# Kernel optimization log

Hardware: AMD Instinct MI355X
Metric: run time of the kernel (lower is better)

The kernel has to match this reference:

```python
import jax, jax.numpy as jnp
import numpy as np

RADIUS = 0.5
HEADS = 4
LATENT = 128
KIN = 3 + 3 + 3 + 1  # q_pos + o_pos + rel + dist
LN_EPS = 1e-5


def setup_inputs() -> dict:
    key = jax.random.key(0)
    ks = jax.random.split(key, 12)
    B, Nq, No = 2, 1024, 1024
    h_obs = jax.random.normal(ks[0], (B, No, LATENT), dtype=jnp.float32)
    pos_obs = jax.random.uniform(ks[1], (B, No, 3), dtype=jnp.float32)
    pos_query = jax.random.uniform(ks[2], (B, Nq, 3), dtype=jnp.float32)
    obs_mask = jax.random.randint(ks[3], (B, No), 0, 2, dtype=jnp.int32)
    # kernel MLP params: Linear(KIN, LATENT) -> ReLU -> Linear(LATENT, HEADS)
    W1 = jax.random.normal(ks[4], (KIN, LATENT), dtype=jnp.float32) * (1.0 / np.sqrt(KIN))
    b1 = jax.random.normal(ks[5], (LATENT,), dtype=jnp.float32) * 0.01
    W2 = jax.random.normal(ks[6], (LATENT, HEADS), dtype=jnp.float32) * (1.0 / np.sqrt(LATENT))
    b2 = jax.random.normal(ks[7], (HEADS,), dtype=jnp.float32) * 0.01
    ln_g = jnp.ones((LATENT,), dtype=jnp.float32)
    ln_b = jnp.zeros((LATENT,), dtype=jnp.float32)
    Wv = jax.random.normal(ks[8], (LATENT, LATENT), dtype=jnp.float32) * (1.0 / np.sqrt(LATENT))
    bv = jax.random.normal(ks[9], (LATENT,), dtype=jnp.float32) * 0.01
    return {"h_obs": h_obs, "pos_obs": pos_obs, "pos_query": pos_query,
            "obs_mask": obs_mask, "W1": W1, "b1": b1, "W2": W2, "b2": b2,
            "ln_g": ln_g, "ln_b": ln_b, "Wv": Wv, "bv": bv}


def reference(h_obs, pos_obs, pos_query, obs_mask, W1, b1, W2, b2, ln_g, ln_b, Wv, bv):
    B, Nq, _ = pos_query.shape
    _, No, _ = pos_obs.shape
    H, D = HEADS, LATENT // HEADS

    # pairwise geometric encoding: (B, Nq, No, *)
    rel = pos_query[:, :, None, :] - pos_obs[:, None, :, :]
    dist = jnp.linalg.norm(rel, axis=-1, keepdims=True)
    q_exp = jnp.broadcast_to(pos_query[:, :, None, :], rel.shape)
    o_exp = jnp.broadcast_to(pos_obs[:, None, :, :], rel.shape)
    kin = jnp.concatenate([q_exp, o_exp, rel, dist], axis=-1)  # (B,Nq,No,KIN)

    # per-pair MLP -> per-head attention logits
    hid = jax.nn.relu(kin @ W1 + b1)                 # (B,Nq,No,LATENT)
    logits = hid @ W2 + b2                           # (B,Nq,No,H)
    logits = jnp.transpose(logits, (0, 3, 1, 2))     # (B,H,Nq,No)

    # radius + observation masking
    neg = jnp.float32(-jnp.inf)
    mask = (dist[..., 0] > RADIUS)[:, None, :, :] | (obs_mask == 0)[:, None, None, :]
    logits = jnp.where(mask, neg, logits)
    weights = jax.nn.softmax(logits, axis=-1)        # (B,H,Nq,No)

    # value path: LayerNorm + projection
    mu = jnp.mean(h_obs, axis=-1, keepdims=True)
    var = jnp.var(h_obs, axis=-1, keepdims=True)
    hn = (h_obs - mu) / jnp.sqrt(var + LN_EPS) * ln_g + ln_b
    v = hn @ Wv + bv                                 # (B,No,LATENT)
    v = jnp.transpose(v.reshape(B, No, H, D), (0, 2, 1, 3))  # (B,H,No,D)

    out = jnp.einsum('bhqo,bhod->bhqd', weights, v)  # (B,H,Nq,D)
    out = jnp.transpose(out, (0, 2, 1, 3)).reshape(B, Nq, H * D)
    return out
```

## Files before the change

### kernel.cpp

```cpp
#include <hip/hip_runtime.h>
#include <math.h>
#include <float.h>

#define B_ 2
#define NQ 1024
#define NO 1024
#define LAT 128
#define NHEADS 4
#define RADIUS_ 0.5f
#define LN_EPS_ 1e-5f

#define V_BYTES ((size_t)B_ * NO * LAT * 4)

__global__ __launch_bounds__(128) void gano_prep_kernel(
    const float* __restrict__ h_obs, const float* __restrict__ ln_g,
    const float* __restrict__ ln_b, const float* __restrict__ Wv,
    const float* __restrict__ bv, const float* __restrict__ W1,
    const float* __restrict__ b1, float* __restrict__ v_out,
    float4* __restrict__ Cw, float4* __restrict__ A4, int write_derived)
{
  const int r = blockIdx.x;
  const int j = threadIdx.x;
  __shared__ float s_red[2];
  __shared__ __align__(16) float s_hn[LAT];

  const float x = h_obs[(size_t)r * LAT + j];

  float s = x;
  #pragma unroll
  for (int off = 32; off >= 1; off >>= 1) s += __shfl_down(s, off);
  if ((j & 63) == 0) s_red[j >> 6] = s;
  __syncthreads();
  const float mu = (s_red[0] + s_red[1]) * (1.0f / LAT);
  const float d = x - mu;
  __syncthreads();
  float s2 = d * d;
  #pragma unroll
  for (int off = 32; off >= 1; off >>= 1) s2 += __shfl_down(s2, off);
  if ((j & 63) == 0) s_red[j >> 6] = s2;
  __syncthreads();
  const float var = (s_red[0] + s_red[1]) * (1.0f / LAT);
  const float rstd = rsqrtf(var + LN_EPS_);
  s_hn[j] = d * rstd * ln_g[j] + ln_b[j];
  __syncthreads();

  float acc = bv[j];
  const float4* hn4 = (const float4*)s_hn;
  #pragma unroll 4
  for (int k4 = 0; k4 < LAT / 4; ++k4) {
    const float4 h4 = hn4[k4];
    acc = fmaf(h4.x, Wv[(k4 * 4 + 0) * LAT + j], acc);
    acc = fmaf(h4.y, Wv[(k4 * 4 + 1) * LAT + j], acc);
    acc = fmaf(h4.z, Wv[(k4 * 4 + 2) * LAT + j], acc);
    acc = fmaf(h4.w, Wv[(k4 * 4 + 3) * LAT + j], acc);
  }
  v_out[(size_t)r * LAT + j] = acc;

  if (write_derived && r == 0) {
    float w[10];
    #pragma unroll
    for (int k = 0; k < 10; ++k) w[k] = W1[k * LAT + j];
    Cw[j] = make_float4(w[3] - w[6], w[4] - w[7], w[5] - w[8], w[9]);
    A4[j] = make_float4(w[0] + w[6], w[1] + w[7], w[2] + w[8], b1[j]);
  }
}

template <bool DERIVED>
__global__ __launch_bounds__(256, 8) void gano_main_kernel(
    const float* __restrict__ pos_obs, const float* __restrict__ pos_query,
    const int* __restrict__ obs_mask,
    const float* __restrict__ W1, const float* __restrict__ b1,
    const float4* __restrict__ W2v, const float* __restrict__ b2,
    const float* __restrict__ v,
    const float4* __restrict__ Cw, const float4* __restrict__ A4,
    float* __restrict__ out)
{
  __shared__ __align__(16) float s_Q[LAT];
  __shared__ int   s_vidx[NO];
  __shared__ float s_vdist[NO];
  __shared__ float s_p[NHEADS][256];
  __shared__ int   s_cnt[16];
  __shared__ float s_red[NHEADS][4];
  __shared__ float s_m[NHEADS];
  __shared__ float s_z[NHEADS];
  __shared__ float s_scale[NHEADS];
  __shared__ float s_acc[LAT];

  const int tid = threadIdx.x;
  const int wave = tid >> 6, lane = tid & 63;
  const int bid = blockIdx.x;
  const int b = bid >> 10, q = bid & (NQ - 1);

  const float qx = pos_query[((size_t)b * NQ + q) * 3 + 0];
  const float qy = pos_query[((size_t)b * NQ + q) * 3 + 1];
  const float qz = pos_query[((size_t)b * NQ + q) * 3 + 2];

  if (tid < LAT) {
    float a0, a1, a2, a3;
    if constexpr (DERIVED) {
      const float4 a = A4[tid];
      a0 = a.x; a1 = a.y; a2 = a.z; a3 = a.w;
    } else {
      a0 = W1[0 * LAT + tid] + W1[6 * LAT + tid];
      a1 = W1[1 * LAT + tid] + W1[7 * LAT + tid];
      a2 = W1[2 * LAT + tid] + W1[8 * LAT + tid];
      a3 = b1[tid];
    }
    s_Q[tid] = fmaf(qx, a0, fmaf(qy, a1, fmaf(qz, a2, a3)));
  }
  if (tid < NHEADS) { s_m[tid] = -FLT_MAX; s_z[tid] = 0.0f; }

  const float* pob = pos_obs + (size_t)b * NO * 3;
  const int*   om  = obs_mask + (size_t)b * NO;
  float dists[4];
  unsigned long long bals[4];
  #pragma unroll
  for (int rd = 0; rd < 4; ++rd) {
    const int o = (rd << 8) + tid;
    const float ox = pob[o * 3 + 0], oy = pob[o * 3 + 1], oz = pob[o * 3 + 2];
    const float rx = qx - ox, ry = qy - oy, rz = qz - oz;
    const float dist = sqrtf(rx * rx + ry * ry + rz * rz);
    const int ok = (om[o] != 0) && (dist <= RADIUS_);
    const unsigned long long bal = __ballot(ok);
    if (lane == 0) s_cnt[(rd << 2) + wave] = __popcll(bal);
    bals[rd] = bal;
    dists[rd] = dist;
  }
  __syncthreads();
  int Nv = 0;
  #pragma unroll
  for (int k = 0; k < 16; ++k) Nv += s_cnt[k];
  #pragma unroll
  for (int rd = 0; rd < 4; ++rd) {
    const int slot = (rd << 2) + wave;
    int base = 0;
    for (int k = 0; k < slot; ++k) base += s_cnt[k];
    if ((bals[rd] >> lane) & 1ull) {
      const int pos = base + __popcll(bals[rd] & ((1ull << lane) - 1ull));
      s_vidx[pos] = (rd << 8) + tid;
      s_vdist[pos] = dists[rd];
    }
  }
  __syncthreads();

  const int col = tid & (LAT - 1);
  const int half = tid >> 7;
  const int hh = col >> 5;
  float acc = 0.0f;
  const float* vb = v + (size_t)b * NO * LAT;
  const float b20 = b2[0], b21 = b2[1], b22 = b2[2], b23 = b2[3];

  const int ntiles = (Nv + 255) >> 8;
  for (int tile = 0; tile < ntiles; ++tile) {
    const int tbase = tile << 8;
    const int t = tbase + tid;
    const bool active = t < Nv;
    float l0 = -FLT_MAX, l1 = -FLT_MAX, l2 = -FLT_MAX, l3 = -FLT_MAX;
    if (__any(active)) {
      const int tt = active ? t : (Nv - 1);
      const int idx = s_vidx[tt];
      const float dist = s_vdist[tt];
      const float ox = pob[idx * 3 + 0], oy = pob[idx * 3 + 1], oz = pob[idx * 3 + 2];
      float a0 = b20, a1 = b21, a2 = b22, a3 = b23;
      for (int j4 = 0; j4 < LAT / 4; ++j4) {
        const float4 q4 = *(const float4*)&s_Q[j4 << 2];
        #pragma unroll
        for (int u = 0; u < 4; ++u) {
          const int j = (j4 << 2) + u;
          float4 cw;
          if constexpr (DERIVED) {
            cw = Cw[j];
          } else {
            cw = make_float4(W1[3 * LAT + j] - W1[6 * LAT + j],
                             W1[4 * LAT + j] - W1[7 * LAT + j],
                             W1[5 * LAT + j] - W1[8 * LAT + j],
                             W1[9 * LAT + j]);
          }
          const float4 w2 = W2v[j];
          const float qj = (u == 0) ? q4.x : (u == 1) ? q4.y : (u == 2) ? q4.z : q4.w;
          float t0 = fmaf(cw.x, ox, qj);
          t0 = fmaf(cw.y, oy, t0);
          t0 = fmaf(cw.z, oz, t0);
          t0 = fmaf(cw.w, dist, t0);
          t0 = fmaxf(t0, 0.0f);
          a0 = fmaf(t0, w2.x, a0);
          a1 = fmaf(t0, w2.y, a1);
          a2 = fmaf(t0, w2.z, a2);
          a3 = fmaf(t0, w2.w, a3);
        }
      }
      if (active) { l0 = a0; l1 = a1; l2 = a2; l3 = a3; }
    }

    float m0 = l0, m1 = l1, m2 = l2, m3 = l3;
    #pragma unroll
    for (int off = 32; off >= 1; off >>= 1) {
      m0 = fmaxf(m0, __shfl_down(m0, off));
      m1 = fmaxf(m1, __shfl_down(m1, off));
      m2 = fmaxf(m2, __shfl_down(m2, off));
      m3 = fmaxf(m3, __shfl_down(m3, off));
    }
    if (lane == 0) { s_red[0][wave] = m0; s_red[1][wave] = m1;
                     s_red[2][wave] = m2; s_red[3][wave] = m3; }
    __syncthreads();
    if (tid < NHEADS) {
      const float tm = fmaxf(fmaxf(s_red[tid][0], s_red[tid][1]),
                             fmaxf(s_red[tid][2], s_red[tid][3]));
      const float om_ = s_m[tid];
      const float nm = fmaxf(om_, tm);
      s_scale[tid] = __expf(om_ - nm);
      s_m[tid] = nm;
    }
    __syncthreads();
    const float nm0 = s_m[0], nm1 = s_m[1], nm2 = s_m[2], nm3 = s_m[3];
    const float p0 = __expf(l0 - nm0);
    const float p1 = __expf(l1 - nm1);
    const float p2 = __expf(l2 - nm2);
    const float p3 = __expf(l3 - nm3);
    s_p[0][tid] = p0; s_p[1][tid] = p1; s_p[2][tid] = p2; s_p[3][tid] = p3;
    float z0 = p0, z1 = p1, z2 = p2, z3 = p3;
    #pragma unroll
    for (int off = 32; off >= 1; off >>= 1) {
      z0 += __shfl_down(z0, off);
      z1 += __shfl_down(z1, off);
      z2 += __shfl_down(z2, off);
      z3 += __shfl_down(z3, off);
    }
    if (lane == 0) { s_red[0][wave] = z0; s_red[1][wave] = z1;
                     s_red[2][wave] = z2; s_red[3][wave] = z3; }
    acc *= s_scale[hh];
    __syncthreads();
    if (tid < NHEADS) {
      s_z[tid] = s_z[tid] * s_scale[tid] +
                 (s_red[tid][0] + s_red[tid][1] + s_red[tid][2] + s_red[tid][3]);
    }
    const int tcnt = min(256, Nv - tbase);
    float aa0 = 0.0f, aa1 = 0.0f;
    int u2 = half;
    for (; u2 + 2 < tcnt; u2 += 4) {
      const float pA = s_p[hh][u2];
      const float pB = s_p[hh][u2 + 2];
      const int iA = s_vidx[tbase + u2];
      const int iB = s_vidx[tbase + u2 + 2];
      aa0 = fmaf(pA, vb[iA * LAT + col], aa0);
      aa1 = fmaf(pB, vb[iB * LAT + col], aa1);
    }
    for (; u2 < tcnt; u2 += 2)
      aa0 = fmaf(s_p[hh][u2], vb[s_vidx[tbase + u2] * LAT + col], aa0);
    acc += aa0 + aa1;
    __syncthreads();
  }

  if (half) s_acc[col] = acc;
  __syncthreads();
  if (!half) {
    float r = 0.0f;
    if (Nv > 0) r = (acc + s_acc[col]) / s_z[hh];
    out[((size_t)b * NQ + q) * LAT + col] = r;
  }
}

extern "C" void kernel_launch(void* const* d_in, const int* in_sizes, int n_in,
                              void* d_out, int out_size, void* d_ws, size_t ws_size,
                              hipStream_t stream) {
  const float* h_obs     = (const float*)d_in[0];
  const float* pos_obs   = (const float*)d_in[1];
  const float* pos_query = (const float*)d_in[2];
  const int*   obs_mask  = (const int*)d_in[3];
  const float* W1        = (const float*)d_in[4];
  const float* b1        = (const float*)d_in[5];
  const float* W2        = (const float*)d_in[6];
  const float* b2        = (const float*)d_in[7];
  const float* ln_g      = (const float*)d_in[8];
  const float* ln_b      = (const float*)d_in[9];
  const float* Wv        = (const float*)d_in[10];
  const float* bv        = (const float*)d_in[11];
  float* outp = (float*)d_out;
  float* v    = (float*)d_ws;

  const size_t need = V_BYTES + 2 * LAT * sizeof(float4);
  const int derived = (ws_size >= need) ? 1 : 0;
  float4* Cw = (float4*)((char*)d_ws + V_BYTES);
  float4* A4 = Cw + LAT;
  if (!derived) { Cw = (float4*)d_ws; A4 = (float4*)d_ws; }

  gano_prep_kernel<<<B_ * NO, 128, 0, stream>>>(h_obs, ln_g, ln_b, Wv, bv,
                                                W1, b1, v, Cw, A4, derived);
  if (derived) {
    gano_main_kernel<true><<<B_ * NQ, 256, 0, stream>>>(
        pos_obs, pos_query, obs_mask, W1, b1, (const float4*)W2, b2, v,
        (const float4*)Cw, (const float4*)A4, outp);
  } else {
    gano_main_kernel<false><<<B_ * NQ, 256, 0, stream>>>(
        pos_obs, pos_query, obs_mask, W1, b1, (const float4*)W2, b2, v,
        (const float4*)Cw, (const float4*)A4, outp);
  }
}
```

Measured before the change: 48.19 us.

## Enlarge softmax tile, vectorize value gather, keep stats in registers, batch LN rows

New measurement: 39.36 us. 18.3% less time.

```diff
diff --git a/kernel.cpp b/kernel.cpp
--- a/kernel.cpp
+++ b/kernel.cpp
@@ -9,64 +9,139 @@
 #define NHEADS 4
 #define RADIUS_ 0.5f
 #define LN_EPS_ 1e-5f
+#define TILE 512
+#define TILE_P (TILE + 8)
 
 #define V_BYTES ((size_t)B_ * NO * LAT * 4)
 
-__global__ __launch_bounds__(128) void gano_prep_kernel(
+__device__ __forceinline__ float selh(int h, float a, float b, float c, float d) {
+  return h == 0 ? a : (h == 1 ? b : (h == 2 ? c : d));
+}
+
+__global__ __launch_bounds__(256) void gano_prep_kernel(
     const float* __restrict__ h_obs, const float* __restrict__ ln_g,
     const float* __restrict__ ln_b, const float* __restrict__ Wv,
     const float* __restrict__ bv, const float* __restrict__ W1,
     const float* __restrict__ b1, float* __restrict__ v_out,
     float4* __restrict__ Cw, float4* __restrict__ A4, int write_derived)
 {
-  const int r = blockIdx.x;
-  const int j = threadIdx.x;
-  __shared__ float s_red[2];
-  __shared__ __align__(16) float s_hn[LAT];
-
-  const float x = h_obs[(size_t)r * LAT + j];
-
-  float s = x;
-  #pragma unroll
-  for (int off = 32; off >= 1; off >>= 1) s += __shfl_down(s, off);
-  if ((j & 63) == 0) s_red[j >> 6] = s;
-  __syncthreads();
-  const float mu = (s_red[0] + s_red[1]) * (1.0f / LAT);
-  const float d = x - mu;
-  __syncthreads();
-  float s2 = d * d;
-  #pragma unroll
-  for (int off = 32; off >= 1; off >>= 1) s2 += __shfl_down(s2, off);
-  if ((j & 63) == 0) s_red[j >> 6] = s2;
-  __syncthreads();
-  const float var = (s_red[0] + s_red[1]) * (1.0f / LAT);
-  const float rstd = rsqrtf(var + LN_EPS_);
-  s_hn[j] = d * rstd * ln_g[j] + ln_b[j];
-  __syncthreads();
-
-  float acc = bv[j];
-  const float4* hn4 = (const float4*)s_hn;
+  const int tid = threadIdx.x;
+  const int j = tid & 127;
+  const int half = tid >> 7;
+  const int wave = tid >> 6;
+  const int lane = tid & 63;
+  const int r0 = blockIdx.x * 4 + half * 2;
+
+  __shared__ float s_redA[2][4];
+  __shared__ float s_redB[2][4];
+  __shared__ __align__(16) float s_hn[4][LAT];
+
+  const float x0 = h_obs[(size_t)r0 * LAT + j];
+  const float x1 = h_obs[(size_t)(r0 + 1) * LAT + j];
+  float s0 = x0, s1 = x1;
+  #pragma unroll
+  for (int off = 32; off >= 1; off >>= 1) {
+    s0 += __shfl_down(s0, off);
+    s1 += __shfl_down(s1, off);
+  }
+  if (lane == 0) { s_redA[0][wave] = s0; s_redA[1][wave] = s1; }
+  __syncthreads();
+  const float mu0 = (s_redA[0][half * 2] + s_redA[0][half * 2 + 1]) * (1.0f / LAT);
+  const float mu1 = (s_redA[1][half * 2] + s_redA[1][half * 2 + 1]) * (1.0f / LAT);
+  const float d0 = x0 - mu0, d1 = x1 - mu1;
+  float q0 = d0 * d0, q1 = d1 * d1;
+  #pragma unroll
+  for (int off = 32; off >= 1; off >>= 1) {
+    q0 += __shfl_down(q0, off);
+    q1 += __shfl_down(q1, off);
+  }
+  if (lane == 0) { s_redB[0][wave] = q0; s_redB[1][wave] = q1; }
+  __syncthreads();
+  const float var0 = (s_redB[0][half * 2] + s_redB[0][half * 2 + 1]) * (1.0f / LAT);
+  const float var1 = (s_redB[1][half * 2] + s_redB[1][half * 2 + 1]) * (1.0f / LAT);
+  const float g = ln_g[j], be = ln_b[j];
+  s_hn[half * 2 + 0][j] = d0 * rsqrtf(var0 + LN_EPS_) * g + be;
+  s_hn[half * 2 + 1][j] = d1 * rsqrtf(var1 + LN_EPS_) * g + be;
+  __syncthreads();
+
+  float a0 = 0.0f, a1 = 0.0f;
+  const float4* h0 = (const float4*)s_hn[half * 2 + 0];
+  const float4* h1 = (const float4*)s_hn[half * 2 + 1];
   #pragma unroll 4
   for (int k4 = 0; k4 < LAT / 4; ++k4) {
-    const float4 h4 = hn4[k4];
-    acc = fmaf(h4.x, Wv[(k4 * 4 + 0) * LAT + j], acc);
-    acc = fmaf(h4.y, Wv[(k4 * 4 + 1) * LAT + j], acc);
-    acc = fmaf(h4.z, Wv[(k4 * 4 + 2) * LAT + j], acc);
-    acc = fmaf(h4.w, Wv[(k4 * 4 + 3) * LAT + j], acc);
-  }
-  v_out[(size_t)r * LAT + j] = acc;
-
-  if (write_derived && r == 0) {
+    const float4 u0 = h0[k4];
+    const float4 u1 = h1[k4];
+    const float w0 = Wv[(k4 * 4 + 0) * LAT + j];
+    const float w1 = Wv[(k4 * 4 + 1) * LAT + j];
+    const float w2 = Wv[(k4 * 4 + 2) * LAT + j];
+    const float w3 = Wv[(k4 * 4 + 3) * LAT + j];
+    a0 = fmaf(u0.x, w0, a0); a0 = fmaf(u0.y, w1, a0);
+    a0 = fmaf(u0.z, w2, a0); a0 = fmaf(u0.w, w3, a0);
+    a1 = fmaf(u1.x, w0, a1); a1 = fmaf(u1.y, w1, a1);
+    a1 = fmaf(u1.z, w2, a1); a1 = fmaf(u1.w, w3, a1);
+  }
+  const float bvj = bv[j];
+  v_out[(size_t)(r0 + 0) * LAT + j] = a0 + bvj;
+  v_out[(size_t)(r0 + 1) * LAT + j] = a1 + bvj;
+
+  if (write_derived && blockIdx.x == 0 && tid < LAT) {
     float w[10];
     #pragma unroll
-    for (int k = 0; k < 10; ++k) w[k] = W1[k * LAT + j];
-    Cw[j] = make_float4(w[3] - w[6], w[4] - w[7], w[5] - w[8], w[9]);
-    A4[j] = make_float4(w[0] + w[6], w[1] + w[7], w[2] + w[8], b1[j]);
+    for (int k = 0; k < 10; ++k) w[k] = W1[k * LAT + tid];
+    Cw[tid] = make_float4(w[3] - w[6], w[4] - w[7], w[5] - w[8], w[9]);
+    A4[tid] = make_float4(w[0] + w[6], w[1] + w[7], w[2] + w[8], b1[tid]);
   }
 }
 
 template <bool DERIVED>
-__global__ __launch_bounds__(256, 8) void gano_main_kernel(
+__device__ __forceinline__ void mlp_logits(
+    int t, int Nv, const float* s_Q, const int* s_vidx, const float* s_vdist,
+    const float* __restrict__ pob, const float4* __restrict__ Cw,
+    const float4* __restrict__ W2v, const float* __restrict__ W1,
+    float b20, float b21, float b22, float b23,
+    float& l0, float& l1, float& l2, float& l3)
+{
+  const bool active = t < Nv;
+  l0 = l1 = l2 = l3 = -FLT_MAX;
+  if (!__any(active)) return;
+  const int tt = active ? t : Nv - 1;
+  const int idx = s_vidx[tt];
+  const float dist = s_vdist[tt];
+  const float ox = pob[idx * 3 + 0], oy = pob[idx * 3 + 1], oz = pob[idx * 3 + 2];
+  float a0 = b20, a1 = b21, a2 = b22, a3 = b23;
+  #pragma unroll 2
+  for (int j4 = 0; j4 < LAT / 4; ++j4) {
+    const float4 q4 = *(const float4*)&s_Q[j4 << 2];
+    #pragma unroll
+    for (int u = 0; u < 4; ++u) {
+      const int jj = (j4 << 2) + u;
+      float4 cw;
+      if constexpr (DERIVED) {
+        cw = Cw[jj];
+      } else {
+        cw = make_float4(W1[3 * LAT + jj] - W1[6 * LAT + jj],
+                         W1[4 * LAT + jj] - W1[7 * LAT + jj],
+                         W1[5 * LAT + jj] - W1[8 * LAT + jj],
+                         W1[9 * LAT + jj]);
+      }
+      const float4 w2 = W2v[jj];
+      const float qj = (u == 0) ? q4.x : (u == 1) ? q4.y : (u == 2) ? q4.z : q4.w;
+      float gg = fmaf(cw.x, ox, qj);
+      gg = fmaf(cw.y, oy, gg);
+      gg = fmaf(cw.z, oz, gg);
+      gg = fmaf(cw.w, dist, gg);
+      gg = fmaxf(gg, 0.0f);
+      a0 = fmaf(gg, w2.x, a0);
+      a1 = fmaf(gg, w2.y, a1);
+      a2 = fmaf(gg, w2.z, a2);
+      a3 = fmaf(gg, w2.w, a3);
+    }
+  }
+  if (active) { l0 = a0; l1 = a1; l2 = a2; l3 = a3; }
+}
+
+template <bool DERIVED>
+__global__ __launch_bounds__(256, 6) void gano_main_kernel(
     const float* __restrict__ pos_obs, const float* __restrict__ pos_query,
     const int* __restrict__ obs_mask,
     const float* __restrict__ W1, const float* __restrict__ b1,
@@ -78,13 +153,11 @@
   __shared__ __align__(16) float s_Q[LAT];
   __shared__ int   s_vidx[NO];
   __shared__ float s_vdist[NO];
-  __shared__ float s_p[NHEADS][256];
+  __shared__ float s_p[NHEADS][TILE_P];
   __shared__ int   s_cnt[16];
   __shared__ float s_red[NHEADS][4];
-  __shared__ float s_m[NHEADS];
-  __shared__ float s_z[NHEADS];
-  __shared__ float s_scale[NHEADS];
-  __shared__ float s_acc[LAT];
+  __shared__ float s_zred[NHEADS][4];
+  __shared__ __align__(16) float s_part[4][LAT];
 
   const int tid = threadIdx.x;
   const int wave = tid >> 6, lane = tid & 63;
@@ -108,7 +181,6 @@
     }
     s_Q[tid] = fmaf(qx, a0, fmaf(qy, a1, fmaf(qz, a2, a3)));
   }
-  if (tid < NHEADS) { s_m[tid] = -FLT_MAX; s_z[tid] = 0.0f; }
 
   const float* pob = pos_obs + (size_t)b * NO * 3;
   const int*   om  = obs_mask + (size_t)b * NO;
@@ -143,120 +215,113 @@
   }
   __syncthreads();
 
-  const int col = tid & (LAT - 1);
-  const int half = tid >> 7;
-  const int hh = col >> 5;
-  float acc = 0.0f;
+  const int c5 = tid & 31;
+  const int phase = tid >> 5;
+  const int hh = c5 >> 3;
+  float ax = 0.f, ay = 0.f, az = 0.f, aw = 0.f;
+  float m0 = -FLT_MAX, m1 = -FLT_MAX, m2 = -FLT_MAX, m3 = -FLT_MAX;
+  float z0 = 0.f, z1 = 0.f, z2 = 0.f, z3 = 0.f;
+  const float b20 = b2[0], b21 = b2[1], b22 = b2[2], b23 = b2[3];
   const float* vb = v + (size_t)b * NO * LAT;
-  const float b20 = b2[0], b21 = b2[1], b22 = b2[2], b23 = b2[3];
-
-  const int ntiles = (Nv + 255) >> 8;
+  const float* vcol = vb + (c5 << 2);
+
+  const int ntiles = (Nv + TILE - 1) >> 9;
   for (int tile = 0; tile < ntiles; ++tile) {
-    const int tbase = tile << 8;
-    const int t = tbase + tid;
-    const bool active = t < Nv;
-    float l0 = -FLT_MAX, l1 = -FLT_MAX, l2 = -FLT_MAX, l3 = -FLT_MAX;
-    if (__any(active)) {
-      const int tt = active ? t : (Nv - 1);
-      const int idx = s_vidx[tt];
-      const float dist = s_vdist[tt];
-      const float ox = pob[idx * 3 + 0], oy = pob[idx * 3 + 1], oz = pob[idx * 3 + 2];
-      float a0 = b20, a1 = b21, a2 = b22, a3 = b23;
-      for (int j4 = 0; j4 < LAT / 4; ++j4) {
-        const float4 q4 = *(const float4*)&s_Q[j4 << 2];
-        #pragma unroll
-        for (int u = 0; u < 4; ++u) {
-          const int j = (j4 << 2) + u;
-          float4 cw;
-          if constexpr (DERIVED) {
-            cw = Cw[j];
-          } else {
-            cw = make_float4(W1[3 * LAT + j] - W1[6 * LAT + j],
-                             W1[4 * LAT + j] - W1[7 * LAT + j],
-                             W1[5 * LAT + j] - W1[8 * LAT + j],
-                             W1[9 * LAT + j]);
-          }
-          const float4 w2 = W2v[j];
-          const float qj = (u == 0) ? q4.x : (u == 1) ? q4.y : (u == 2) ? q4.z : q4.w;
-          float t0 = fmaf(cw.x, ox, qj);
-          t0 = fmaf(cw.y, oy, t0);
-          t0 = fmaf(cw.z, oz, t0);
-          t0 = fmaf(cw.w, dist, t0);
-          t0 = fmaxf(t0, 0.0f);
-          a0 = fmaf(t0, w2.x, a0);
-          a1 = fmaf(t0, w2.y, a1);
-          a2 = fmaf(t0, w2.z, a2);
-          a3 = fmaf(t0, w2.w, a3);
-        }
-      }
-      if (active) { l0 = a0; l1 = a1; l2 = a2; l3 = a3; }
-    }
-
-    float m0 = l0, m1 = l1, m2 = l2, m3 = l3;
+    const int tbase = tile << 9;
+    float l00, l01, l02, l03, l10, l11, l12, l13;
+    mlp_logits<DERIVED>(tbase + tid, Nv, s_Q, s_vidx, s_vdist, pob, Cw, W2v, W1,
+                        b20, b21, b22, b23, l00, l01, l02, l03);
+    mlp_logits<DERIVED>(tbase + 256 + tid, Nv, s_Q, s_vidx, s_vdist, pob, Cw, W2v, W1,
+                        b20, b21, b22, b23, l10, l11, l12, l13);
+
+    float t0 = fmaxf(l00, l10), t1 = fmaxf(l01, l11);
+    float t2 = fmaxf(l02, l12), t3 = fmaxf(l03, l13);
     #pragma unroll
     for (int off = 32; off >= 1; off >>= 1) {
-      m0 = fmaxf(m0, __shfl_down(m0, off));
-      m1 = fmaxf(m1, __shfl_down(m1, off));
-      m2 = fmaxf(m2, __shfl_down(m2, off));
-      m3 = fmaxf(m3, __shfl_down(m3, off));
-    }
-    if (lane == 0) { s_red[0][wave] = m0; s_red[1][wave] = m1;
-                     s_red[2][wave] = m2; s_red[3][wave] = m3; }
+      t0 = fmaxf(t0, __shfl_down(t0, off));
+      t1 = fmaxf(t1, __shfl_down(t1, off));
+      t2 = fmaxf(t2, __shfl_down(t2, off));
+      t3 = fmaxf(t3, __shfl_down(t3, off));
+    }
+    if (lane == 0) { s_red[0][wave] = t0; s_red[1][wave] = t1;
+                     s_red[2][wave] = t2; s_red[3][wave] = t3; }
     __syncthreads();
-    if (tid < NHEADS) {
-      const float tm = fmaxf(fmaxf(s_red[tid][0], s_red[tid][1]),
-                             fmaxf(s_red[tid][2], s_red[tid][3]));
-      const float om_ = s_m[tid];
-      const float nm = fmaxf(om_, tm);
-      s_scale[tid] = __expf(om_ - nm);
-      s_m[tid] = nm;
-    }
-    __syncthreads();
-    const float nm0 = s_m[0], nm1 = s_m[1], nm2 = s_m[2], nm3 = s_m[3];
-    const float p0 = __expf(l0 - nm0);
-    const float p1 = __expf(l1 - nm1);
-    const float p2 = __expf(l2 - nm2);
-    const float p3 = __expf(l3 - nm3);
-    s_p[0][tid] = p0; s_p[1][tid] = p1; s_p[2][tid] = p2; s_p[3][tid] = p3;
-    float z0 = p0, z1 = p1, z2 = p2, z3 = p3;
+    const float x0 = fmaxf(fmaxf(s_red[0][0], s_red[0][1]), fmaxf(s_red[0][2], s_red[0][3]));
+    const float x1 = fmaxf(fmaxf(s_red[1][0], s_red[1][1]), fmaxf(s_red[1][2], s_red[1][3]));
+    const float x2 = fmaxf(fmaxf(s_red[2][0], s_red[2][1]), fmaxf(s_red[2][2], s_red[2][3]));
+    const float x3 = fmaxf(fmaxf(s_red[3][0], s_red[3][1]), fmaxf(s_red[3][2], s_red[3][3]));
+    const float nm0 = fmaxf(m0, x0), nm1 = fmaxf(m1, x1);
+    const float nm2 = fmaxf(m2, x2), nm3 = fmaxf(m3, x3);
+    const float sc0 = __expf(m0 - nm0), sc1 = __expf(m1 - nm1);
+    const float sc2 = __expf(m2 - nm2), sc3 = __expf(m3 - nm3);
+    m0 = nm0; m1 = nm1; m2 = nm2; m3 = nm3;
+
+    const float p00 = __expf(l00 - nm0), p01 = __expf(l01 - nm1);
+    const float p02 = __expf(l02 - nm2), p03 = __expf(l03 - nm3);
+    const float p10 = __expf(l10 - nm0), p11 = __expf(l11 - nm1);
+    const float p12 = __expf(l12 - nm2), p13 = __expf(l13 - nm3);
+    s_p[0][tid] = p00; s_p[0][256 + tid] = p10;
+    s_p[1][tid] = p01; s_p[1][256 + tid] = p11;
+    s_p[2][tid] = p02; s_p[2][256 + tid] = p12;
+    s_p[3][tid] = p03; s_p[3][256 + tid] = p13;
+    float u0 = p00 + p10, u1 = p01 + p11, u2 = p02 + p12, u3 = p03 + p13;
     #pragma unroll
     for (int off = 32; off >= 1; off >>= 1) {
-      z0 += __shfl_down(z0, off);
-      z1 += __shfl_down(z1, off);
-      z2 += __shfl_down(z2, off);
-      z3 += __shfl_down(z3, off);
-    }
-    if (lane == 0) { s_red[0][wave] = z0; s_red[1][wave] = z1;
-                     s_red[2][wave] = z2; s_red[3][wave] = z3; }
-    acc *= s_scale[hh];
+      u0 += __shfl_down(u0, off);
+      u1 += __shfl_down(u1, off);
+      u2 += __shfl_down(u2, off);
+      u3 += __shfl_down(u3, off);
+    }
+    if (lane == 0) { s_zred[0][wave] = u0; s_zred[1][wave] = u1;
+                     s_zred[2][wave] = u2; s_zred[3][wave] = u3; }
     __syncthreads();
-    if (tid < NHEADS) {
-      s_z[tid] = s_z[tid] * s_scale[tid] +
-                 (s_red[tid][0] + s_red[tid][1] + s_red[tid][2] + s_red[tid][3]);
-    }
-    const int tcnt = min(256, Nv - tbase);
-    float aa0 = 0.0f, aa1 = 0.0f;
-    int u2 = half;
-    for (; u2 + 2 < tcnt; u2 += 4) {
-      const float pA = s_p[hh][u2];
-      const float pB = s_p[hh][u2 + 2];
-      const int iA = s_vidx[tbase + u2];
-      const int iB = s_vidx[tbase + u2 + 2];
-      aa0 = fmaf(pA, vb[iA * LAT + col], aa0);
-      aa1 = fmaf(pB, vb[iB * LAT + col], aa1);
-    }
-    for (; u2 < tcnt; u2 += 2)
-      aa0 = fmaf(s_p[hh][u2], vb[s_vidx[tbase + u2] * LAT + col], aa0);
-    acc += aa0 + aa1;
-    __syncthreads();
-  }
-
-  if (half) s_acc[col] = acc;
-  __syncthreads();
-  if (!half) {
-    float r = 0.0f;
-    if (Nv > 0) r = (acc + s_acc[col]) / s_z[hh];
-    out[((size_t)b * NQ + q) * LAT + col] = r;
+    z0 = z0 * sc0 + (s_zred[0][0] + s_zred[0][1] + s_zred[0][2] + s_zred[0][3]);
+    z1 = z1 * sc1 + (s_zred[1][0] + s_zred[1][1] + s_zred[1][2] + s_zred[1][3]);
+    z2 = z2 * sc2 + (s_zred[2][0] + s_zred[2][1] + s_zred[2][2] + s_zred[2][3]);
+    z3 = z3 * sc3 + (s_zred[3][0] + s_zred[3][1] + s_zred[3][2] + s_zred[3][3]);
+    const float scme = selh(hh, sc0, sc1, sc2, sc3);
+    ax *= scme; ay *= scme; az *= scme; aw *= scme;
+
+    const int tcnt = min(TILE, Nv - tbase);
+    int it = phase;
+    float bx = 0.f, by = 0.f, bz = 0.f, bw = 0.f;
+    for (; it + 8 < tcnt; it += 16) {
+      const float pA = s_p[hh][it];
+      const float pB = s_p[hh][it + 8];
+      const int iA = s_vidx[tbase + it];
+      const int iB = s_vidx[tbase + it + 8];
+      const float4 vA = *(const float4*)(vcol + (size_t)iA * LAT);
+      const float4 vB = *(const float4*)(vcol + (size_t)iB * LAT);
+      ax = fmaf(pA, vA.x, ax); ay = fmaf(pA, vA.y, ay);
+      az = fmaf(pA, vA.z, az); aw = fmaf(pA, vA.w, aw);
+      bx = fmaf(pB, vB.x, bx); by = fmaf(pB, vB.y, by);
+      bz = fmaf(pB, vB.z, bz); bw = fmaf(pB, vB.w, bw);
+    }
+    if (it < tcnt) {
+      const float pA = s_p[hh][it];
+      const int iA = s_vidx[tbase + it];
+      const float4 vA = *(const float4*)(vcol + (size_t)iA * LAT);
+      ax = fmaf(pA, vA.x, ax); ay = fmaf(pA, vA.y, ay);
+      az = fmaf(pA, vA.z, az); aw = fmaf(pA, vA.w, aw);
+    }
+    ax += bx; ay += by; az += bz; aw += bw;
+    if (tile + 1 < ntiles) __syncthreads();
+  }
+
+  ax += __shfl_down(ax, 32);
+  ay += __shfl_down(ay, 32);
+  az += __shfl_down(az, 32);
+  aw += __shfl_down(aw, 32);
+  if (lane < 32) {
+    *(float4*)&s_part[wave][lane << 2] = make_float4(ax, ay, az, aw);
+  }
+  __syncthreads();
+  if (tid < LAT) {
+    const float r4 = s_part[0][tid] + s_part[1][tid] + s_part[2][tid] + s_part[3][tid];
+    const int h = tid >> 5;
+    const float zz = selh(h, z0, z1, z2, z3);
+    const float r = (Nv > 0) ? (r4 / zz) : 0.0f;
+    out[((size_t)b * NQ + q) * LAT + tid] = r;
   }
 }
 
@@ -284,8 +349,8 @@
   float4* A4 = Cw + LAT;
   if (!derived) { Cw = (float4*)d_ws; A4 = (float4*)d_ws; }
 
-  gano_prep_kernel<<<B_ * NO, 128, 0, stream>>>(h_obs, ln_g, ln_b, Wv, bv,
-                                                W1, b1, v, Cw, A4, derived);
+  gano_prep_kernel<<<(B_ * NO) / 4, 256, 0, stream>>>(h_obs, ln_g, ln_b, Wv, bv,
+                                                      W1, b1, v, Cw, A4, derived);
   if (derived) {
     gano_main_kernel<true><<<B_ * NQ, 256, 0, stream>>>(
         pos_obs, pos_query, obs_mask, W1, b1, (const float4*)W2, b2, v,
```
